# Performance work log

Hardware: AMD Instinct MI355X
Metric: run time of the kernel (lower is better)

## Reference

```python
import jax, jax.numpy as jnp
import numpy as np
from jax import lax

V, E, H, M, B, L = 4000, 256, 256, 128, 32, 4
PUNC, ENG, NUM, EOS = 0, 1, 2, 3
LOGINF = 1000000.0


def _lstm(xs, h0, c0, Wih, Whh, bih, bhh):
    # xs: [T, N, H]; single-layer torch LSTM, gate order i,f,g,o
    def step(carry, x):
        h, c = carry
        g = x @ Wih.T + bih + h @ Whh.T + bhh
        i, f, gg, o = jnp.split(g, 4, axis=-1)
        c = jax.nn.sigmoid(f) * c + jax.nn.sigmoid(i) * jnp.tanh(gg)
        h = jax.nn.sigmoid(o) * jnp.tanh(c)
        return (h, c), h
    _, hs = lax.scan(step, (h0, c0), xs)
    return hs


def _forward(x, lengths, embedding, e2v_b, enc_Wih, enc_Whh, enc_bih, enc_bhh,
             enc_h0, enc_c0, dec_Wih, dec_Whh, dec_bih, dec_bhh,
             dht_W, dht_b, sos_W, sos_b):
    xT = x.T  # [M, B]
    inputs = embedding[xT]  # [M, B, H]
    is_single = ((xT == PUNC) | (xT == ENG) | (xT == NUM)).astype(jnp.float32) * (-LOGINF)  # [M, B]

    # context encoder (learned init states broadcast over batch), output halved
    h0 = jnp.broadcast_to(enc_h0, (B, H))
    c0 = jnp.broadcast_to(enc_c0, (B, H))
    enc_out = _lstm(inputs, h0, c0, enc_Wih, enc_Whh, enc_bih, enc_bhh) * 0.5  # [M, B, H]

    S = M - 2
    starts = jnp.arange(1, M - 1)  # [S] segment start positions
    enc_prev = enc_out[starts - 1]  # [S, B, H]
    sos = enc_prev @ sos_W.T + sos_b                       # start-of-segment symbol [S,B,H]
    dec_h0 = jnp.tanh(enc_prev @ dht_W.T + dht_b)          # decoder h init (1 layer) [S,B,H]
    dec_c0 = jnp.zeros_like(dec_h0)

    pad_in = jnp.concatenate([inputs, jnp.zeros((L, B, H), inputs.dtype)], axis=0)  # [M+L,B,H]
    idx = starts[:, None] + jnp.arange(L)[None, :]  # [S, L] token positions j_start+t
    seg_in = pad_in[idx]  # [S, L, B, H]
    dec_in = jnp.concatenate([sos[:, None], seg_in], axis=1)  # [S, L+1, B, H]
    dec_in = dec_in.transpose(1, 0, 2, 3).reshape(L + 1, S * B, H)
    dec_out = _lstm(dec_in, dec_h0.reshape(S * B, H), dec_c0.reshape(S * B, H),
                    dec_Wih, dec_Whh, dec_bih, dec_bhh).reshape(L + 1, S, B, H)

    logits = jnp.einsum('tsbh,vh->tsbv', dec_out, embedding) + e2v_b  # tied e2v weight
    logp = jax.nn.log_softmax(logits, axis=-1)  # [L+1, S, B, V]

    x_pad = jnp.concatenate([xT, jnp.zeros((L, B), xT.dtype)], axis=0)
    tgt = x_pad[idx]  # [S, L, B]
    lp_t = logp[:L].transpose(1, 0, 2, 3)  # [S, L, B, V]
    tlp = jnp.take_along_axis(lp_t, tgt[..., None].astype(jnp.int32), axis=-1)[..., 0]  # [S,L,B]

    is_pad = jnp.concatenate([is_single, jnp.zeros((L, B), jnp.float32)], axis=0)
    seg_is = is_pad[idx]  # is_single[j_start+t], [S,L,B]
    kge1 = (jnp.arange(L) >= 1).astype(jnp.float32)[None, :, None]  # t>=1 mask
    cum = jnp.cumsum(tlp + seg_is * kge1, axis=1)
    cum = cum + kge1 * is_single[starts][:, None, :]  # add is_single[j_start] once from k==1 on

    eos_lp = logp[1:, :, :, EOS].transpose(1, 0, 2)  # [S, L, B]
    logpy_seg = cum + eos_lp
    j_len = jnp.minimum(L, (M - 1) - starts)  # [S]
    kvalid = jnp.arange(L)[None, :] < j_len[:, None]
    logpy_seg = jnp.where(kvalid[:, :, None], logpy_seg, -LOGINF)

    row0 = jnp.full((1, L, B), -LOGINF, jnp.float32).at[0, 0].set(0.0)
    logpy = jnp.concatenate([row0, logpy_seg], axis=0)  # [M-1, L, B]

    # seg_lp[e, d-1] = logpy[j_start+1 = e-(d-1)][d-1] for segment length d ending at e
    e_idx = jnp.arange(M - 1)[:, None] - jnp.arange(L)[None, :]  # [M-1, L]
    gathered = logpy[jnp.clip(e_idx, 0, M - 2), jnp.arange(L)[None, :]]  # [M-1, L, B]
    seg_lp = jnp.where((e_idx >= 1)[:, :, None], gathered, -LOGINF)

    def dp_step(buf, lp_e):  # buf[d-1] = alpha[e-d], [L, B]
        a = jax.scipy.special.logsumexp(buf + lp_e, axis=0)  # [B]
        return jnp.concatenate([a[None], buf[:-1]], axis=0), a

    buf0 = jnp.full((L, B), -LOGINF, jnp.float32).at[0].set(0.0)  # alpha[0]=0
    _, alphas_rest = lax.scan(dp_step, buf0, seg_lp[1:])  # e = 1..M-2
    alphas = jnp.concatenate([jnp.zeros((1, B), jnp.float32), alphas_rest], axis=0)  # [M-1, B]

    nll = -alphas[lengths - 2, jnp.arange(B)]
    total = jnp.sum(lengths) - 2 * B
    return jnp.sum(nll) / total.astype(jnp.float32)


def setup_inputs() -> dict:
    key = jax.random.key(0)
    ks = jax.random.split(key, 16)
    w = lambda k, shape: (jax.random.normal(k, shape, jnp.float32) * 0.05)
    return {
        'x': jax.random.randint(ks[0], (B, M), 0, V, jnp.int32),
        'lengths': jnp.full((B,), M, jnp.int32),
        'embedding': jax.random.uniform(ks[1], (V, E), jnp.float32, -1.0, 1.0),
        'e2v_b': w(ks[2], (V,)),
        'enc_Wih': w(ks[3], (4 * H, H)),
        'enc_Whh': w(ks[4], (4 * H, H)),
        'enc_bih': w(ks[5], (4 * H,)),
        'enc_bhh': w(ks[6], (4 * H,)),
        'enc_h0': jnp.zeros((1, H), jnp.float32),
        'enc_c0': jnp.zeros((1, H), jnp.float32),
        'dec_Wih': w(ks[7], (4 * H, H)),
        'dec_Whh': w(ks[8], (4 * H, H)),
        'dec_bih': w(ks[9], (4 * H,)),
        'dec_bhh': w(ks[10], (4 * H,)),
        'dht_W': w(ks[11], (H, H)),
        'dht_b': w(ks[12], (H,)),
        'sos_W': w(ks[13], (H, H)),
        'sos_b': w(ks[14], (H,)),
    }


def reference(x, lengths, embedding, e2v_b, enc_Wih, enc_Whh, enc_bih, enc_bhh,
              enc_h0, enc_c0, dec_Wih, dec_Whh, dec_bih, dec_bhh,
              dht_W, dht_b, sos_W, sos_b):
    return _forward(x, lengths, embedding, e2v_b, enc_Wih, enc_Whh, enc_bih, enc_bhh,
                    enc_h0, enc_c0, dec_Wih, dec_Whh, dec_bih, dec_bhh,
                    dht_W, dht_b, sos_W, sos_b)
```

## Files before the change

### kernel.cpp

```cpp
#include <hip/hip_runtime.h>
#include <math.h>


#define LOGNEG -1000000.0f
#define GF_BIAS 1
#define GF_TANH 2
#define GF_F16OUT 16
#define ZSHIFT 8.0f

typedef unsigned int uint32;
typedef _Float16 half2_t __attribute__((ext_vector_type(2)));
typedef _Float16 half8_t __attribute__((ext_vector_type(8)));
typedef float    f32x4_t __attribute__((ext_vector_type(4)));

__device__ __forceinline__ float sigmf_(float x){ return 1.0f/(1.0f+expf(-x)); }

__device__ __forceinline__ float dot2f(uint32 w, uint32 h, float acc){
#if __has_builtin(__builtin_amdgcn_fdot2)
    return __builtin_amdgcn_fdot2(__builtin_bit_cast(half2_t, w),
                                  __builtin_bit_cast(half2_t, h), acc, false);
#else
    half2_t a = __builtin_bit_cast(half2_t, w);
    half2_t b = __builtin_bit_cast(half2_t, h);
    return acc + (float)a[0]*(float)b[0] + (float)a[1]*(float)b[1];
#endif
}

__device__ __forceinline__ void gemm16_body(
    _Float16* Bs, int tid,
    const _Float16* __restrict__ A, const _Float16* __restrict__ W,
    const float* __restrict__ bias, float* __restrict__ C,
    _Float16* __restrict__ C16, int N, int flags, int rowBlk, int colBlk)
{
    int wave = tid >> 6, lane = tid & 63;
    int ln = lane & 15, quad = lane >> 4;
    half8_t a[8];
    if (tid < 256){
        #pragma unroll
        for (int i = 0; i < 8; i++){
            int idx = i*256 + tid;
            int row = idx >> 5, c16 = idx & 31;
            *(uint4*)&Bs[row*264 + c16*8] =
                *(const uint4*)(W + (size_t)(colBlk+row)*256 + c16*8);
        }
        const half8_t* Ap = (const half8_t*)(A + (size_t)(rowBlk + wave*16 + ln)*256 + quad*8);
        #pragma unroll
        for (int ks = 0; ks < 8; ks++) a[ks] = Ap[ks*4];
    }
    __syncthreads();
    if (tid < 256){
        #pragma unroll
        for (int ct = 0; ct < 4; ct++){
            f32x4_t c4 = {0.f,0.f,0.f,0.f};
            const _Float16* bp = &Bs[(ct*16+ln)*264 + quad*8];
            #pragma unroll
            for (int ks = 0; ks < 8; ks++){
                half8_t b = *(const half8_t*)(bp + ks*32);
                c4 = __builtin_amdgcn_mfma_f32_16x16x32_f16(a[ks], b, c4, 0, 0, 0);
            }
            int c = colBlk + ct*16 + ln;
            #pragma unroll
            for (int reg = 0; reg < 4; reg++){
                int r = rowBlk + wave*16 + quad*4 + reg;
                float v = c4[reg];
                if (flags & GF_BIAS) v += bias[c];
                if (flags & GF_TANH) v = tanhf(v);
                if (flags & GF_F16OUT) C16[(size_t)r*N + c] = (_Float16)v;
                else                   C  [(size_t)r*N + c] = v;
            }
        }
    }
}

__global__ __launch_bounds__(256) void k_prep(
    const int* __restrict__ x,
    const float* __restrict__ emb, const float* __restrict__ e2v_b,
    const float* __restrict__ eWih, const float* __restrict__ dWih,
    const float* __restrict__ dWhh, const float* __restrict__ eWhh,
    const float* __restrict__ sosW, const float* __restrict__ dhtW,
    const float* __restrict__ ebih, const float* __restrict__ ebhh,
    const float* __restrict__ dbih, const float* __restrict__ dbhh,
    _Float16* __restrict__ emb16, float* __restrict__ biasOff,
    _Float16* __restrict__ dWih16, _Float16* __restrict__ dWhh16,
    _Float16* __restrict__ eWhh16, _Float16* __restrict__ sosW16,
    _Float16* __restrict__ dhtW16, float* __restrict__ bias_d,
    _Float16* __restrict__ emb_in16, float* __restrict__ is_s,
    _Float16* __restrict__ XgE16)
{
    __shared__ _Float16 Bs[64*264];
    int bx = blockIdx.x, tid = threadIdx.x;
    if (bx < 1465){
        #pragma unroll 1
        for (int rr = 0; rr < 8; rr++){
            int v = bx*8 + rr;
            if (v >= 11716) break;
            if (v < 4032){
                int row = v;
                emb16[(size_t)row*256 + tid] = (row < 4000) ? (_Float16)emb[(size_t)row*256 + tid] : (_Float16)0.0f;
                if (tid == 0) biasOff[row] = (row < 4000) ? (e2v_b[row] - ZSHIFT) : -200.0f;
            } else if (v < 5056){
                int r = v - 4032; dWih16[(size_t)r*256 + tid] = (_Float16)dWih[(size_t)r*256 + tid];
            } else if (v < 6080){
                int r = v - 5056; dWhh16[(size_t)r*256 + tid] = (_Float16)dWhh[(size_t)r*256 + tid];
            } else if (v < 7104){
                int r = v - 6080; eWhh16[(size_t)r*256 + tid] = (_Float16)eWhh[(size_t)r*256 + tid];
            } else if (v < 7360){
                int r = v - 7104; sosW16[(size_t)r*256 + tid] = (_Float16)sosW[(size_t)r*256 + tid];
            } else if (v < 7616){
                int r = v - 7360; dhtW16[(size_t)r*256 + tid] = (_Float16)dhtW[(size_t)r*256 + tid];
            } else if (v < 7620){
                int j = (v - 7616)*256 + tid;
                if (j < 1024) bias_d[j] = dbih[j] + dbhh[j];
            } else {
                int ri = v - 7620;
                int m = ri >> 5, b = ri & 31;
                int tok = x[b*128 + m];
                emb_in16[(size_t)ri*256 + tid] = (_Float16)emb[(size_t)tok*256 + tid];
                if (tid == 0) is_s[ri] = (tok <= 2) ? LOGNEG : 0.0f;
            }
        }
    } else {
        int tile = bx - 1465;
        int rowBlk = (tile >> 4)*64, colBlk = (tile & 15)*64;
        #pragma unroll
        for (int i = 0; i < 8; i++){
            int idx = i*256 + tid;
            int row = idx >> 5, c16 = idx & 31;
            const float* src = eWih + (size_t)(colBlk+row)*256 + c16*8;
            float4 f0 = *(const float4*)src;
            float4 f1 = *(const float4*)(src + 4);
            half8_t hv;
            hv[0]=(_Float16)f0.x; hv[1]=(_Float16)f0.y; hv[2]=(_Float16)f0.z; hv[3]=(_Float16)f0.w;
            hv[4]=(_Float16)f1.x; hv[5]=(_Float16)f1.y; hv[6]=(_Float16)f1.z; hv[7]=(_Float16)f1.w;
            *(half8_t*)&Bs[row*264 + c16*8] = hv;
        }
        int wave = tid >> 6, lane = tid & 63;
        int ln = lane & 15, quad = lane >> 4;
        int r = rowBlk + wave*16 + ln;
        int m = r >> 5, b_ = r & 31;
        int tok = x[b_*128 + m];
        half8_t a[8];
        #pragma unroll
        for (int ks = 0; ks < 8; ks++){
            const float* ap = emb + (size_t)tok*256 + quad*8 + ks*32;
            float4 f0 = *(const float4*)ap;
            float4 f1 = *(const float4*)(ap + 4);
            half8_t hv;
            hv[0]=(_Float16)f0.x; hv[1]=(_Float16)f0.y; hv[2]=(_Float16)f0.z; hv[3]=(_Float16)f0.w;
            hv[4]=(_Float16)f1.x; hv[5]=(_Float16)f1.y; hv[6]=(_Float16)f1.z; hv[7]=(_Float16)f1.w;
            a[ks] = hv;
        }
        __syncthreads();
        #pragma unroll
        for (int ct = 0; ct < 4; ct++){
            f32x4_t c4 = {0.f,0.f,0.f,0.f};
            const _Float16* bp = &Bs[(ct*16+ln)*264 + quad*8];
            #pragma unroll
            for (int ks = 0; ks < 8; ks++){
                half8_t b = *(const half8_t*)(bp + ks*32);
                c4 = __builtin_amdgcn_mfma_f32_16x16x32_f16(a[ks], b, c4, 0, 0, 0);
            }
            int c = colBlk + ct*16 + ln;
            float bb = ebih[c] + ebhh[c];
            #pragma unroll
            for (int reg = 0; reg < 4; reg++){
                int rr2 = rowBlk + wave*16 + quad*4 + reg;
                XgE16[(size_t)rr2*1024 + c] = (_Float16)(c4[reg] + bb);
            }
        }
    }
}

__global__ void __attribute__((amdgpu_flat_work_group_size(512,512), amdgpu_waves_per_eu(2,2)))
k_enc_rnn(
    const _Float16* __restrict__ Xg16, const _Float16* __restrict__ Whh16,
    const float* __restrict__ h0, const float* __restrict__ c0,
    _Float16* __restrict__ enc_out16,
    const _Float16* __restrict__ emb_in16, const _Float16* __restrict__ dWih16,
    const float* __restrict__ bias_d, _Float16* __restrict__ Xg16dec)
{
    extern __shared__ char smem[];
    const int bx = blockIdx.x, tid = threadIdx.x;
    if (bx >= 32){
        int eng = tid >> 8, ltid = tid & 255;
        _Float16* Bs = (_Float16*)smem + (size_t)eng*(64*264);
        int base = (bx - 32)*2 + eng;
        for (int rnd = 0; rnd < 3; rnd++){
            int tile = rnd*448 + base;
            __syncthreads();
            if (tile < 1024)
                gemm16_body(Bs, ltid, emb_in16, dWih16, bias_d, nullptr, Xg16dec,
                            1024, GF_BIAS|GF_F16OUT, (tile >> 4)*64, (tile & 15)*64);
            else
                __syncthreads();
        }
        return;
    }
    uint4*     wlds = (uint4*)smem;
    _Float16*  hb   = (_Float16*)(smem + 147456);
    const int b = bx;
    const int w_ = tid >> 6, l_ = tid & 63;
    const int u  = w_*32 + (l_ & 31);
    const int hi = l_ >> 5;
    const int rA = hi*512 + u;
    const int rB = rA + 256;

    const uint4* pA = (const uint4*)(Whh16 + (size_t)rA*256);
    const uint4* pB = (const uint4*)(Whh16 + (size_t)rB*256);
    uint4 wA[23], wB[23];
    #pragma unroll
    for (int i = 0; i < 23; i++){ wA[i] = pA[i]; wB[i] = pB[i]; }
    #pragma unroll
    for (int i = 0; i < 9; i++){
        wlds[(i*2 + 0)*512 + tid] = pA[23 + i];
        wlds[(i*2 + 1)*512 + tid] = pB[23 + i];
    }
    float c = c0[u];
    if (tid < 256) hb[tid] = (_Float16)h0[tid];
    __syncthreads();

    float xgA = (float)Xg16[(size_t)b*1024 + rA];
    float xgB = (float)Xg16[(size_t)b*1024 + rB];

    for (int t = 0; t < 128; t++){
        const int cur = t & 1, nxt = cur ^ 1;
        float nxgA = 0.f, nxgB = 0.f;
        if (t < 127){
            const _Float16* xp = Xg16 + ((size_t)((t+1)*32 + b))*1024;
            nxgA = (float)xp[rA]; nxgB = (float)xp[rB];
        }
        const uint4* hu4 = (const uint4*)(hb + cur*256);
        float aA = 0.f, aB = 0.f;
        #pragma unroll
        for (int i = 0; i < 23; i++){
            uint4 hh = hu4[i];
            aA = dot2f(wA[i].x, hh.x, aA); aA = dot2f(wA[i].y, hh.y, aA);
            aA = dot2f(wA[i].z, hh.z, aA); aA = dot2f(wA[i].w, hh.w, aA);
            aB = dot2f(wB[i].x, hh.x, aB); aB = dot2f(wB[i].y, hh.y, aB);
            aB = dot2f(wB[i].z, hh.z, aB); aB = dot2f(wB[i].w, hh.w, aB);
        }
        #pragma unroll
        for (int i = 0; i < 9; i++){
            uint4 hh = hu4[23 + i];
            uint4 vA = wlds[(i*2 + 0)*512 + tid];
            uint4 vB = wlds[(i*2 + 1)*512 + tid];
            aA = dot2f(vA.x, hh.x, aA); aA = dot2f(vA.y, hh.y, aA);
            aA = dot2f(vA.z, hh.z, aA); aA = dot2f(vA.w, hh.w, aA);
            aB = dot2f(vB.x, hh.x, aB); aB = dot2f(vB.y, hh.y, aB);
            aB = dot2f(vB.z, hh.z, aB); aB = dot2f(vB.w, hh.w, aB);
        }
        float gA = aA + xgA, gB = aB + xgB;
        float oA = __shfl_xor(gA, 32, 64);
        float oB = __shfl_xor(gB, 32, 64);
        float gi = hi ? oA : gA;
        float gf = hi ? oB : gB;
        float gg = hi ? gA : oA;
        float go = hi ? gB : oB;
        c = sigmf_(gf)*c + sigmf_(gi)*tanhf(gg);
        float hn = sigmf_(go)*tanhf(c);
        if (!hi){
            enc_out16[((size_t)(t*32 + b))*256 + u] = (_Float16)(0.5f*hn);
            hb[nxt*256 + u] = (_Float16)hn;
        }
        __syncthreads();
        xgA = nxgA; xgB = nxgB;
    }
}

__global__ __launch_bounds__(256) void k_head(
    const _Float16* __restrict__ enc_out16,
    const _Float16* __restrict__ sosW16, const float* __restrict__ sos_b, _Float16* __restrict__ sos16,
    const _Float16* __restrict__ dhtW16, const float* __restrict__ dht_b, _Float16* __restrict__ dech0_16)
{
    __shared__ _Float16 Bs[64*264];
    int z = blockIdx.z;
    gemm16_body(Bs, threadIdx.x, enc_out16,
                z ? dhtW16 : sosW16, z ? dht_b : sos_b, nullptr,
                z ? dech0_16 : sos16, 256,
                z ? (GF_BIAS|GF_TANH|GF_F16OUT) : (GF_BIAS|GF_F16OUT),
                blockIdx.y*64, blockIdx.x*64);
}

__global__ __launch_bounds__(256) void k_dec_step(
    const _Float16* __restrict__ hprev, const _Float16* __restrict__ sosA,
    const _Float16* __restrict__ dWhh16, const _Float16* __restrict__ dWih16,
    const _Float16* __restrict__ base16, const float* __restrict__ bias_d,
    float* __restrict__ dec_c, _Float16* __restrict__ dec16_j, int jstep)
{
    __shared__ _Float16 Bs[64*264];
    int tid = threadIdx.x;
    int wave = tid >> 6, lane = tid & 63;
    int ln = lane & 15, quad = lane >> 4;
    int u0 = blockIdx.x * 64, r0 = blockIdx.y * 64;

    half8_t aH[8], aS[8];
    {
        const half8_t* Ap = (const half8_t*)(hprev + (size_t)(r0 + wave*16 + ln)*256 + quad*8);
        #pragma unroll
        for (int ks = 0; ks < 8; ks++) aH[ks] = Ap[ks*4];
    }
    if (jstep == 0){
        const half8_t* Ap = (const half8_t*)(sosA + (size_t)(r0 + wave*16 + ln)*256 + quad*8);
        #pragma unroll
        for (int ks = 0; ks < 8; ks++) aS[ks] = Ap[ks*4];
    }

    f32x4_t cg[4][4];
    #pragma unroll
    for (int g = 0; g < 4; g++){
        int colBlk = g*256 + u0;
        __syncthreads();
        #pragma unroll
        for (int i = 0; i < 8; i++){
            int idx = i*256 + tid;
            int row = idx >> 5, c16 = idx & 31;
            *(uint4*)&Bs[row*264 + c16*8] =
                *(const uint4*)(dWhh16 + (size_t)(colBlk+row)*256 + c16*8);
        }
        __syncthreads();
        #pragma unroll
        for (int ct = 0; ct < 4; ct++){
            f32x4_t c4 = {0.f,0.f,0.f,0.f};
            const _Float16* bp = &Bs[(ct*16+ln)*264 + quad*8];
            #pragma unroll
            for (int ks = 0; ks < 8; ks++){
                half8_t b = *(const half8_t*)(bp + ks*32);
                c4 = __builtin_amdgcn_mfma_f32_16x16x32_f16(aH[ks], b, c4, 0, 0, 0);
            }
            cg[g][ct] = c4;
        }
        if (jstep == 0){
            __syncthreads();
            #pragma unroll
            for (int i = 0; i < 8; i++){
                int idx = i*256 + tid;
                int row = idx >> 5, c16 = idx & 31;
                *(uint4*)&Bs[row*264 + c16*8] =
                    *(const uint4*)(dWih16 + (size_t)(colBlk+row)*256 + c16*8);
            }
            __syncthreads();
            #pragma unroll
            for (int ct = 0; ct < 4; ct++){
                f32x4_t c4 = cg[g][ct];
                const _Float16* bp = &Bs[(ct*16+ln)*264 + quad*8];
                #pragma unroll
                for (int ks = 0; ks < 8; ks++){
                    half8_t b = *(const half8_t*)(bp + ks*32);
                    c4 = __builtin_amdgcn_mfma_f32_16x16x32_f16(aS[ks], b, c4, 0, 0, 0);
                }
                cg[g][ct] = c4;
            }
        }
    }
    #pragma unroll
    for (int ct = 0; ct < 4; ct++){
        int u = u0 + ct*16 + ln;
        #pragma unroll
        for (int reg = 0; reg < 4; reg++){
            int r = r0 + wave*16 + quad*4 + reg;
            float bi, bf, bg, bo;
            if (jstep == 0){
                bi = bias_d[u]; bf = bias_d[256+u]; bg = bias_d[512+u]; bo = bias_d[768+u];
            } else {
                int s = r >> 5, b_ = r & 31;
                int m = s + jstep;
                if (m < 128){
                    const _Float16* bp2 = base16 + (size_t)(m*32+b_)*1024 + u;
                    bi = (float)bp2[0]; bf = (float)bp2[256]; bg = (float)bp2[512]; bo = (float)bp2[768];
                } else {
                    bi = bias_d[u]; bf = bias_d[256+u]; bg = bias_d[512+u]; bo = bias_d[768+u];
                }
            }
            float gi = cg[0][ct][reg] + bi;
            float gf = cg[1][ct][reg] + bf;
            float gg = cg[2][ct][reg] + bg;
            float go = cg[3][ct][reg] + bo;
            float cv = (jstep == 0) ? 0.0f : dec_c[(size_t)r*256 + u];
            cv = sigmf_(gf)*cv + sigmf_(gi)*tanhf(gg);
            float hv = sigmf_(go)*tanhf(cv);
            dec_c[(size_t)r*256 + u] = cv;
            dec16_j[(size_t)r*256 + u] = (_Float16)hv;
        }
    }
}

__global__ __launch_bounds__(256) void k_logits(
    const _Float16* __restrict__ dec16, const _Float16* __restrict__ emb16,
    const float* __restrict__ biasOff, float* __restrict__ ps)
{
    __shared__ _Float16 Bs[64*264];
    int tid = threadIdx.x;
    int wave = tid >> 6, lane = tid & 63;
    int ln = lane & 15, quad = lane >> 4;
    int r0 = blockIdx.x * 128;
    int q = blockIdx.y;
    int vt0 = q*16, vt1 = (q == 3) ? 63 : (vt0 + 16);

    half8_t aA[8], aB[8];
    {
        int ra = r0 + wave*16 + ln;        if (ra >= 20160) ra = 20159;
        int rb = r0 + 64 + wave*16 + ln;   if (rb >= 20160) rb = 20159;
        const half8_t* Ap = (const half8_t*)(dec16 + (size_t)ra*256 + quad*8);
        const half8_t* Bp = (const half8_t*)(dec16 + (size_t)rb*256 + quad*8);
        #pragma unroll
        for (int ks = 0; ks < 8; ks++){ aA[ks] = Ap[ks*4]; aB[ks] = Bp[ks*4]; }
    }

    float sA[4] = {0.f,0.f,0.f,0.f}, sB[4] = {0.f,0.f,0.f,0.f};

    for (int vt = vt0; vt < vt1; vt++){
        int v0 = vt*64;
        __syncthreads();
        #pragma unroll
        for (int i = 0; i < 8; i++){
            int idx = i*256 + tid;
            int row = idx >> 5, c16 = idx & 31;
            *(uint4*)&Bs[row*264 + c16*8] =
                *(const uint4*)(emb16 + (size_t)(v0+row)*256 + c16*8);
        }
        __syncthreads();

        #pragma unroll
        for (int ct = 0; ct < 4; ct++){
            f32x4_t cA = {0.f,0.f,0.f,0.f}, cB = {0.f,0.f,0.f,0.f};
            const _Float16* bp = &Bs[(ct*16+ln)*264 + quad*8];
            #pragma unroll
            for (int ks = 0; ks < 8; ks++){
                half8_t b = *(const half8_t*)(bp + ks*32);
                cA = __builtin_amdgcn_mfma_f32_16x16x32_f16(aA[ks], b, cA, 0, 0, 0);
                cB = __builtin_amdgcn_mfma_f32_16x16x32_f16(aB[ks], b, cB, 0, 0, 0);
            }
            int vv = v0 + ct*16 + ln;
            float bb = biasOff[vv];
            #pragma unroll
            for (int reg = 0; reg < 4; reg++){
                sA[reg] += __expf(cA[reg] + bb);
                sB[reg] += __expf(cB[reg] + bb);
            }
        }
    }
    #pragma unroll
    for (int reg = 0; reg < 4; reg++){
        float vsA = sA[reg], vsB = sB[reg];
        #pragma unroll
        for (int off = 1; off < 16; off <<= 1){
            vsA += __shfl_xor(vsA, off, 64);
            vsB += __shfl_xor(vsB, off, 64);
        }
        if (ln == 0){
            int rA = r0 + wave*16 + quad*4 + reg;
            int rB = rA + 64;
            if (rA < 20160) ps[q*20160+rA] = vsA;
            if (rB < 20160) ps[q*20160+rB] = vsB;
        }
    }
}

__global__ __launch_bounds__(256) void k_comb_fin(
    const float* __restrict__ ps,
    const _Float16* __restrict__ dec16, const _Float16* __restrict__ emb16,
    const float* __restrict__ biasOff, const int* __restrict__ x,
    const float* __restrict__ is_s, const int* __restrict__ lengths,
    float* __restrict__ tlp, float* __restrict__ eosb,
    float* __restrict__ seg_g, float* __restrict__ out,
    unsigned int* __restrict__ counter)
{
    extern __shared__ float csm[];
    float* tlp_s  = csm;
    float* eosb_s = csm + 16128;
    float* iss_s  = csm + 32256;

    int tid = threadIdx.x;
    int r = blockIdx.x*256 + tid;
    if (r < 20160){
        float lse = __logf(ps[r] + ps[20160+r] + ps[2*20160+r] + ps[3*20160+r]);
        int t = r / 4032, sb = r % 4032;
        int s_ = sb >> 5, b = sb & 31;
        int m = s_ + 1 + t;
        int tg = (m < 128) ? x[b*128 + m] : 0;
        const uint4* dp = (const uint4*)(dec16 + (size_t)r*256);
        const uint4* ep = (const uint4*)(emb16 + (size_t)tg*256);
        const uint4* e3 = (const uint4*)(emb16 + (size_t)3*256);
        float zt = 0.f, ze = 0.f;
        #pragma unroll
        for (int i = 0; i < 32; i++){
            uint4 d = dp[i], e = ep[i], f = e3[i];
            zt = dot2f(d.x, e.x, zt); zt = dot2f(d.y, e.y, zt);
            zt = dot2f(d.z, e.z, zt); zt = dot2f(d.w, e.w, zt);
            ze = dot2f(d.x, f.x, ze); ze = dot2f(d.y, f.y, ze);
            ze = dot2f(d.z, f.z, ze); ze = dot2f(d.w, f.w, ze);
        }
        zt += biasOff[tg];
        ze += biasOff[3];
        if (t < 4)  tlp[(t*126+s_)*32 + b]      = zt - lse;
        if (t >= 1) eosb[((t-1)*126+s_)*32 + b] = ze - lse;
    }
    __threadfence();
    __syncthreads();
    __shared__ int lastBlk;
    if (tid == 0){
        unsigned old = __hip_atomic_fetch_add(counter, 1u, __ATOMIC_ACQ_REL,
                                              __HIP_MEMORY_SCOPE_AGENT);
        lastBlk = (old == 78) ? 1 : 0;
    }
    __syncthreads();
    if (!lastBlk) return;
    __threadfence();

    for (int i = tid; i < 16128; i += 256){
        tlp_s[i]  = tlp[i];
        eosb_s[i] = eosb[i];
    }
    for (int i = tid; i < 4096; i += 256) iss_s[i] = is_s[i];
    __syncthreads();

    int k = tid >> 5, b = tid & 31;
    if (tid < 128){
        for (int s = 0; s < 126; s++){
            float cum = 0.f;
            for (int kk = 0; kk <= k; kk++) cum += tlp_s[(kk*126+s)*32 + b];
            if (k >= 1){
                for (int kk = 1; kk <= k; kk++){
                    int m = s+1+kk;
                    if (m < 128) cum += iss_s[m*32+b];
                }
                cum += iss_s[(s+1)*32 + b];
            }
            float lp = cum + eosb_s[(k*126+s)*32 + b];
            int jl = min(4, 126 - s);
            if (k >= jl) lp = LOGNEG;
            seg_g[(s*4+k)*32 + b] = lp;
        }
    }
    __threadfence_block();
    __syncthreads();
    __shared__ float nll_s[32];
    if (tid < 32){
        int target = lengths[tid] - 2;
        float b0 = 0.f, b1 = LOGNEG, b2 = LOGNEG, b3 = LOGNEG;
        float nllb = 0.f;
        for (int e = 1; e <= 126; e++){
            float v0 = b0 + seg_g[((e-1)*4+0)*32 + tid];
            float v1 = b1 + ((e >= 2) ? seg_g[((e-2)*4+1)*32 + tid] : LOGNEG);
            float v2 = b2 + ((e >= 3) ? seg_g[((e-3)*4+2)*32 + tid] : LOGNEG);
            float v3 = b3 + ((e >= 4) ? seg_g[((e-4)*4+3)*32 + tid] : LOGNEG);
            float mx = fmaxf(fmaxf(v0,v1), fmaxf(v2,v3));
            float a = mx + logf(expf(v0-mx)+expf(v1-mx)+expf(v2-mx)+expf(v3-mx));
            if (e == target) nllb = -a;
            b3 = b2; b2 = b1; b1 = b0; b0 = a;
        }
        nll_s[tid] = nllb;
    }
    __syncthreads();
    if (tid == 0){
        float tot = 0.f; int lsum = 0;
        for (int i = 0; i < 32; i++){ tot += nll_s[i]; lsum += lengths[i]; }
        out[0] = tot / (float)(lsum - 64);
    }
}

extern "C" void kernel_launch(void* const* d_in, const int* in_sizes, int n_in,
                              void* d_out, int out_size, void* d_ws, size_t ws_size,
                              hipStream_t stream)
{
    const int*   x        = (const int*)  d_in[0];
    const int*   lengths  = (const int*)  d_in[1];
    const float* emb      = (const float*)d_in[2];
    const float* e2v_b    = (const float*)d_in[3];
    const float* enc_Wih  = (const float*)d_in[4];
    const float* enc_Whh  = (const float*)d_in[5];
    const float* enc_bih  = (const float*)d_in[6];
    const float* enc_bhh  = (const float*)d_in[7];
    const float* enc_h0   = (const float*)d_in[8];
    const float* enc_c0   = (const float*)d_in[9];
    const float* dec_Wih  = (const float*)d_in[10];
    const float* dec_Whh  = (const float*)d_in[11];
    const float* dec_bih  = (const float*)d_in[12];
    const float* dec_bhh  = (const float*)d_in[13];
    const float* dht_W    = (const float*)d_in[14];
    const float* dht_b    = (const float*)d_in[15];
    const float* sos_W    = (const float*)d_in[16];
    const float* sos_b    = (const float*)d_in[17];
    float* out = (float*)d_out;

    char* wsb = (char*)d_ws;
    size_t off = 0;
    auto alloc = [&](size_t bytes)->void*{
        void* p = (void*)(wsb + off);
        off += ((bytes + 255)/256)*256;
        return p;
    };
    _Float16* emb16    = (_Float16*)alloc((size_t)4032*256*2);
    _Float16* dWih16   = (_Float16*)alloc((size_t)1024*256*2);
    _Float16* dWhh16   = (_Float16*)alloc((size_t)1024*256*2);
    _Float16* eWhh16   = (_Float16*)alloc((size_t)1024*256*2);
    _Float16* sosW16   = (_Float16*)alloc((size_t)256*256*2);
    _Float16* dhtW16   = (_Float16*)alloc((size_t)256*256*2);
    _Float16* emb_in16 = (_Float16*)alloc((size_t)4096*256*2);
    _Float16* XgE16    = (_Float16*)alloc((size_t)4096*1024*2);
    _Float16* Xgdec16  = (_Float16*)alloc((size_t)4096*1024*2);
    _Float16* enc_out16= (_Float16*)alloc((size_t)4096*256*2);
    _Float16* sos16    = (_Float16*)alloc((size_t)4032*256*2);
    _Float16* dech0_16 = (_Float16*)alloc((size_t)4032*256*2);
    _Float16* dec16    = (_Float16*)alloc((size_t)5*4032*256*2);
    float*    dec_c    = (float*)alloc((size_t)4032*256*4);
    float*    biasOff  = (float*)alloc(4032*4);
    float*    bias_d   = (float*)alloc(1024*4);
    float*    is_s     = (float*)alloc(4096*4);
    float*    ps       = (float*)alloc((size_t)4*20160*4);
    float*    tlp      = (float*)alloc((size_t)4*126*32*4);
    float*    eosb     = (float*)alloc((size_t)4*126*32*4);
    float*    seg_g    = (float*)alloc((size_t)126*4*32*4);
    unsigned int* counter = (unsigned int*)alloc(256);
    (void)ws_size; (void)in_sizes; (void)n_in; (void)out_size;

    hipFuncSetAttribute(reinterpret_cast<const void*>(k_enc_rnn),
                        hipFuncAttributeMaxDynamicSharedMemorySize, 148480);
    hipFuncSetAttribute(reinterpret_cast<const void*>(k_comb_fin),
                        hipFuncAttributeMaxDynamicSharedMemorySize, 145408);

    hipMemsetAsync(counter, 0, sizeof(unsigned int), stream);
    k_prep<<<2489, 256, 0, stream>>>(x, emb, e2v_b, enc_Wih, dec_Wih, dec_Whh, enc_Whh,
        sos_W, dht_W, enc_bih, enc_bhh, dec_bih, dec_bhh,
        emb16, biasOff, dWih16, dWhh16, eWhh16, sosW16, dhtW16, bias_d,
        emb_in16, is_s, XgE16);
    k_enc_rnn<<<256, 512, 148480, stream>>>(XgE16, eWhh16, enc_h0, enc_c0, enc_out16,
        emb_in16, dWih16, bias_d, Xgdec16);
    k_head<<<dim3(4,63,2), 256, 0, stream>>>(enc_out16, sosW16, sos_b, sos16,
        dhtW16, dht_b, dech0_16);
    for (int j = 0; j < 5; j++){
        const _Float16* hA = (j == 0) ? dech0_16 : (dec16 + (size_t)(j-1)*4032*256);
        k_dec_step<<<dim3(4,63), 256, 0, stream>>>(hA, sos16, dWhh16, dWih16,
            Xgdec16, bias_d, dec_c, dec16 + (size_t)j*4032*256, j);
    }
    k_logits<<<dim3(158,4), 256, 0, stream>>>(dec16, emb16, biasOff, ps);
    k_comb_fin<<<79, 256, 145408, stream>>>(ps, dec16, emb16, biasOff, x, is_s, lengths,
        tlp, eosb, seg_g, out, counter);
}
```

Baseline: 656.9 us.

## Fuse head GEMMs and five decoder steps into one persistent kernel

Replaces the k_head launch and the five k_dec_step launches with a single kernel, k_hdec, of 63 blocks of 1024 threads. Each block owns a 64-row slice, and its four 256-thread groups each handle 64 hidden units. The sos and dht projections and all decoder steps run in sequence inside the block, with __syncthreads between phases, which removes six launch boundaries. In exchange the grid shrinks from 252 (or 504) small blocks to 63 large ones. That may underfill a GPU with many CUs and reduce latency hiding.

Measured after the change: 841.2 us. 1.28x slower.

```diff
diff --git a/kernel.cpp b/kernel.cpp
--- a/kernel.cpp
+++ b/kernel.cpp
@@ -267,31 +267,16 @@
     }
 }
 
-__global__ __launch_bounds__(256) void k_head(
-    const _Float16* __restrict__ enc_out16,
-    const _Float16* __restrict__ sosW16, const float* __restrict__ sos_b, _Float16* __restrict__ sos16,
-    const _Float16* __restrict__ dhtW16, const float* __restrict__ dht_b, _Float16* __restrict__ dech0_16)
-{
-    __shared__ _Float16 Bs[64*264];
-    int z = blockIdx.z;
-    gemm16_body(Bs, threadIdx.x, enc_out16,
-                z ? dhtW16 : sosW16, z ? dht_b : sos_b, nullptr,
-                z ? dech0_16 : sos16, 256,
-                z ? (GF_BIAS|GF_TANH|GF_F16OUT) : (GF_BIAS|GF_F16OUT),
-                blockIdx.y*64, blockIdx.x*64);
-}
-
-__global__ __launch_bounds__(256) void k_dec_step(
+__device__ __forceinline__ void dec_once(
+    _Float16* Bs, int tid,
     const _Float16* __restrict__ hprev, const _Float16* __restrict__ sosA,
     const _Float16* __restrict__ dWhh16, const _Float16* __restrict__ dWih16,
     const _Float16* __restrict__ base16, const float* __restrict__ bias_d,
-    float* __restrict__ dec_c, _Float16* __restrict__ dec16_j, int jstep)
-{
-    __shared__ _Float16 Bs[64*264];
-    int tid = threadIdx.x;
+    float* __restrict__ dec_c, _Float16* __restrict__ dec16_j,
+    int jstep, int u0, int r0)
+{
     int wave = tid >> 6, lane = tid & 63;
     int ln = lane & 15, quad = lane >> 4;
-    int u0 = blockIdx.x * 64, r0 = blockIdx.y * 64;
 
     half8_t aH[8], aS[8];
     {
@@ -381,6 +366,36 @@
             dec_c[(size_t)r*256 + u] = cv;
             dec16_j[(size_t)r*256 + u] = (_Float16)hv;
         }
+    }
+}
+
+__global__ void __attribute__((amdgpu_flat_work_group_size(1024,1024)))
+k_hdec(
+    const _Float16* __restrict__ enc_out16,
+    const _Float16* __restrict__ sosW16, const float* __restrict__ sos_b, _Float16* __restrict__ sos16,
+    const _Float16* __restrict__ dhtW16, const float* __restrict__ dht_b, _Float16* __restrict__ dech0_16,
+    const _Float16* __restrict__ dWhh16, const _Float16* __restrict__ dWih16,
+    const _Float16* __restrict__ Xgdec16, const float* __restrict__ bias_d,
+    float* __restrict__ dec_c, _Float16* __restrict__ dec16)
+{
+    extern __shared__ char smem[];
+    const int bid = blockIdx.x, tid = threadIdx.x;
+    const int eng = tid >> 8, ltid = tid & 255;
+    _Float16* Bs = (_Float16*)smem + (size_t)eng*(64*264);
+    const int r0 = bid*64, u0 = eng*64;
+
+    gemm16_body(Bs, ltid, enc_out16, sosW16, sos_b, nullptr, sos16,
+                256, GF_BIAS|GF_F16OUT, r0, u0);
+    __syncthreads();
+    gemm16_body(Bs, ltid, enc_out16, dhtW16, dht_b, nullptr, dech0_16,
+                256, GF_BIAS|GF_TANH|GF_F16OUT, r0, u0);
+    __syncthreads();
+
+    for (int j = 0; j < 5; j++){
+        const _Float16* hA = (j == 0) ? dech0_16 : (dec16 + (size_t)(j-1)*4032*256);
+        dec_once(Bs, ltid, hA, sos16, dWhh16, dWih16, Xgdec16, bias_d,
+                 dec_c, dec16 + (size_t)j*4032*256, j, u0, r0);
+        __syncthreads();
     }
 }
 
@@ -616,6 +631,8 @@
 
     hipFuncSetAttribute(reinterpret_cast<const void*>(k_enc_rnn),
                         hipFuncAttributeMaxDynamicSharedMemorySize, 148480);
+    hipFuncSetAttribute(reinterpret_cast<const void*>(k_hdec),
+                        hipFuncAttributeMaxDynamicSharedMemorySize, 135168);
     hipFuncSetAttribute(reinterpret_cast<const void*>(k_comb_fin),
                         hipFuncAttributeMaxDynamicSharedMemorySize, 145408);
 
@@ -626,13 +643,9 @@
         emb_in16, is_s, XgE16);
     k_enc_rnn<<<256, 512, 148480, stream>>>(XgE16, eWhh16, enc_h0, enc_c0, enc_out16,
         emb_in16, dWih16, bias_d, Xgdec16);
-    k_head<<<dim3(4,63,2), 256, 0, stream>>>(enc_out16, sosW16, sos_b, sos16,
-        dhtW16, dht_b, dech0_16);
-    for (int j = 0; j < 5; j++){
-        const _Float16* hA = (j == 0) ? dech0_16 : (dec16 + (size_t)(j-1)*4032*256);
-        k_dec_step<<<dim3(4,63), 256, 0, stream>>>(hA, sos16, dWhh16, dWih16,
-            Xgdec16, bias_d, dec_c, dec16 + (size_t)j*4032*256, j);
-    }
+    k_hdec<<<63, 1024, 135168, stream>>>(enc_out16,
+        sosW16, sos_b, sos16, dhtW16, dht_b, dech0_16,
+        dWhh16, dWih16, Xgdec16, bias_d, dec_c, dec16);
     k_logits<<<dim3(158,4), 256, 0, stream>>>(dec16, emb16, biasOff, ps);
     k_comb_fin<<<79, 256, 145408, stream>>>(ps, dec16, emb16, biasOff, x, is_s, lengths,
         tlp, eosb, seg_g, out, counter);
```
